# Performance work log

Measured on AMD Instinct MI355X. Metric: run time of the kernel, lower is better.

Reference implementation:

```python
import jax, jax.numpy as jnp
import numpy as np

N_QUBITS = 12
N_LAYERS = 3
HID = 16
IN_DIM = 6
BATCH = 4096
C64 = jnp.complex64


def _ry(t):
    c = jnp.cos(t / 2).astype(C64)
    s = jnp.sin(t / 2).astype(C64)
    return jnp.stack([jnp.stack([c, -s], -1), jnp.stack([s, c], -1)], -2)


def _rx(t):
    c = jnp.cos(t / 2).astype(C64)
    s = jnp.sin(t / 2).astype(C64)
    js = 1j * s
    return jnp.stack([jnp.stack([c, -js], -1), jnp.stack([-js, c], -1)], -2)


def _rz(t):
    e = jnp.exp(-1j * t.astype(C64) / 2)
    z = jnp.zeros_like(e)
    return jnp.stack([jnp.stack([e, z], -1), jnp.stack([z, jnp.conj(e)], -1)], -2)


def _apply_1q(state, U, wire):
    # state: (B,) + (2,)*n ; U: (2,2) shared or (B,2,2) per-sample
    s = jnp.moveaxis(state, wire + 1, 1)
    if U.ndim == 2:
        s = jnp.einsum('ij,bj...->bi...', U, s)
    else:
        s = jnp.einsum('bij,bj...->bi...', U, s)
    return jnp.moveaxis(s, 1, wire + 1)


def _cnot(state, c, t):
    ax_c = c + 1
    s0 = jnp.take(state, 0, axis=ax_c)
    s1 = jnp.take(state, 1, axis=ax_c)
    t_ax = t + 1 if t < c else t  # target axis after removing control axis
    s1 = jnp.flip(s1, axis=t_ax)  # X on target when control=1
    return jnp.stack([s0, s1], axis=ax_c)


def _quantum(angles, qparams):
    # angles: (B, n_qubits) angle-encoding RY rotations; qparams: (L, n, 3)
    B = angles.shape[0]
    n = N_QUBITS
    state = jnp.zeros((B,) + (2,) * n, C64).at[(slice(None),) + (0,) * n].set(1.0)
    for i in range(n):
        state = _apply_1q(state, _ry(angles[:, i]), i)
    for l in range(N_LAYERS):
        for i in range(n):
            # RX then RY then RZ on wire i -> fused 2x2
            U = _rz(qparams[l, i, 2]) @ _ry(qparams[l, i, 1]) @ _rx(qparams[l, i, 0])
            state = _apply_1q(state, U, i)
        for i in range(n - 1):
            state = _cnot(state, i, i + 1)
        if n > 2:
            state = _cnot(state, n - 1, 0)
    p = state.real ** 2 + state.imag ** 2  # (B,) + (2,)*n
    evs = []
    for i in range(n):
        axes = tuple(a for a in range(1, n + 1) if a != i + 1)
        pi = p.sum(axes)  # (B, 2)
        evs.append(pi[:, 0] - pi[:, 1])
    return jnp.stack(evs, axis=1)  # (B, n) PauliZ expvals


def setup_inputs() -> dict:
    key = jax.random.key(0)
    ks = jax.random.split(key, 14)
    w = lambda k, shape: jax.random.normal(k, shape, jnp.float32) * 0.1
    return {
        'x': jax.random.normal(ks[0], (BATCH, IN_DIM), jnp.float32),
        'W1': w(ks[1], (HID, IN_DIM)), 'b1': w(ks[2], (HID,)),
        'W2': w(ks[3], (HID, HID)), 'b2': w(ks[4], (HID,)),
        'W3': w(ks[5], (N_QUBITS, HID)), 'b3': w(ks[6], (N_QUBITS,)),
        'qparams': w(ks[7], (N_LAYERS, N_QUBITS, 3)),
        'P1': w(ks[8], (HID, N_QUBITS)), 'c1': w(ks[9], (HID,)),
        'P2': w(ks[10], (8, HID)), 'c2': w(ks[11], (8,)),
        'P3': w(ks[12], (1, 8)), 'c3': w(ks[13], (1,)),
    }


def reference(x, W1, b1, W2, b2, W3, b3, qparams, P1, c1, P2, c2, P3, c3):
    # classical preprocessor (dropout = identity at inference)
    h = jax.nn.relu(x @ W1.T + b1)
    h = jax.nn.relu(h @ W2.T + b2)
    angles = h @ W3.T + b3  # (B, n_qubits)
    q = _quantum(angles, qparams)  # (B, n_qubits)
    # classical postprocessor
    o = jax.nn.relu(q @ P1.T + c1)
    o = jax.nn.relu(o @ P2.T + c2)
    o = jax.nn.sigmoid(o @ P3.T + c3)
    return o.squeeze(-1)  # (B,)
```

## Files before the change

### kernel.cpp

```cpp
#include <hip/hip_runtime.h>
#include <stdint.h>

#define NQ   12
#define DIM  4096
#define TPB  256

typedef float   v2f   __attribute__((ext_vector_type(2)));
typedef float   v4f   __attribute__((ext_vector_type(4)));
typedef float   f32x4 __attribute__((ext_vector_type(4)));
typedef _Float16 v2h  __attribute__((ext_vector_type(2)));
typedef _Float16 f16x8 __attribute__((ext_vector_type(8)));
typedef uint32_t u32x4 __attribute__((ext_vector_type(4)));

struct PassP {
  uint16_t v[4];
  uint16_t m[4];
  uint16_t td[4];
  uint8_t  np[8];
  uint8_t  wire[4];
  uint8_t  layer;
  uint8_t  pad[3];
};
struct ROC {
  uint16_t mask[12];
  uint8_t  bin[12];
};

constexpr int chbit(uint32_t x) { int b = -1; for (int i = 0; i < 32; ++i) if ((x >> i) & 1u) b = i; return b; }

constexpr void bmm(uint32_t* C, const uint32_t* A, const uint32_t* B) {
  for (int i = 0; i < NQ; ++i) {
    uint32_t r = 0;
    for (int j = 0; j < NQ; ++j) if ((A[i] >> j) & 1u) r ^= B[j];
    C[i] = r;
  }
}
constexpr void binv(const uint32_t* M, uint32_t* Inv) {
  uint32_t A[NQ] = {}, I[NQ] = {};
  for (int i = 0; i < NQ; ++i) { A[i] = M[i]; I[i] = 1u << i; }
  for (int c = 0; c < NQ; ++c) {
    int piv = -1;
    for (int r = c; r < NQ; ++r) if ((A[r] >> c) & 1u) { piv = r; break; }
    if (piv < 0) continue;
    uint32_t ta = A[c]; A[c] = A[piv]; A[piv] = ta;
    uint32_t ti = I[c]; I[c] = I[piv]; I[piv] = ti;
    for (int r = 0; r < NQ; ++r)
      if (r != c && ((A[r] >> c) & 1u)) { A[r] ^= A[c]; I[r] ^= I[c]; }
  }
  for (int i = 0; i < NQ; ++i) Inv[i] = I[i];
}

constexpr int rank5(const uint32_t* cols, int n) {
  uint32_t rows[5] = {}; int rnk = 0;
  for (int q = 0; q < n; ++q) {
    uint32_t x = cols[q] & 31u;
    for (int bit = 4; bit >= 0; --bit) {
      if (!((x >> bit) & 1u)) continue;
      if (rows[bit]) { x ^= rows[bit]; }
      else { rows[bit] = x; ++rnk; break; }
    }
  }
  return rnk;
}
constexpr int penalty(int r) {
  return r >= 5 ? 0 : r == 4 ? 58 : r == 3 ? 194 : r == 2 ? 469 : 1100;
}

constexpr PassP make_pass(int p) {
  PassP pp{};
  uint32_t A[NQ] = {}; A[0] = 0xFFEu;
  for (int i = 1; i < NQ; ++i) A[i] = (1u << (i + 1)) - 1u;
  uint32_t A2[NQ] = {}, Ai[NQ] = {}, A2i[NQ] = {};
  bmm(A2, A, A);
  binv(A, Ai); binv(A2, A2i);

  const int L = (p < 3) ? 1 : 2;
  const int wb = (p % 3) * 4;
  const uint32_t* M  = (L == 1) ? A  : A2;
  const uint32_t* Mi = (L == 1) ? Ai : A2i;
  uint32_t v0[4] = {}, m0[4] = {};
  for (int i = 0; i < 4; ++i) {
    int w = wb + i; uint32_t col = 0;
    for (int r = 0; r < NQ; ++r) col |= ((Mi[r] >> w) & 1u) << r;
    v0[i] = col; m0[i] = M[w];
  }
  uint32_t Bc[NQ] = {};
  for (int b = 0; b < NQ; ++b) {
    uint32_t col = 1u << b;
    for (int i = 0; i < 4; ++i) if ((m0[i] >> b) & 1u) col ^= v0[i];
    Bc[b] = col;
  }
  uint32_t redv[4] = {}; int pbit[4] = {}; uint32_t pivmask = 0;
  for (int i = 0; i < 4; ++i) {
    redv[i] = v0[i];
    for (int k2 = 0; k2 < i; ++k2) if ((redv[i] >> pbit[k2]) & 1u) redv[i] ^= redv[k2];
    pbit[i] = chbit(redv[i]); pivmask |= 1u << pbit[i];
  }
  uint8_t np0[8] = {}; int nc = 0;
  for (int b = 0; b < NQ; ++b) if (!((pivmask >> b) & 1u)) np0[nc++] = (uint8_t)b;

  int bestCost = 1 << 30;
  int bsel[4] = {0, 1, 2, 3}; int bperm[4] = {0, 1, 2, 3};
  for (int a = 0; a < 8; ++a) for (int b = a + 1; b < 8; ++b)
  for (int c = b + 1; c < 8; ++c) for (int d = c + 1; d < 8; ++d) {
    uint32_t jc[4] = {Bc[np0[a]], Bc[np0[b]], Bc[np0[c]], Bc[np0[d]]};
    int prk[4][4] = {};
    for (int i = 0; i < 4; ++i)
      for (int j = i + 1; j < 4; ++j) {
        uint32_t sp[6] = {jc[0], jc[1], jc[2], jc[3], v0[i], v0[j]};
        prk[i][j] = prk[j][i] = rank5(sp, 6);
      }
    for (int pa = 0; pa < 4; ++pa) for (int pb2 = 0; pb2 < 4; ++pb2) {
      if (pb2 == pa) continue;
      for (int pc = 0; pc < 4; ++pc) {
        if (pc == pa || pc == pb2) continue;
        const int pd = 6 - pa - pb2 - pc;
        const int cost = penalty(prk[pc][pd]) + penalty(prk[pb2][pc]);
        if (cost < bestCost) {
          bestCost = cost;
          bsel[0] = a; bsel[1] = b; bsel[2] = c; bsel[3] = d;
          bperm[0] = pa; bperm[1] = pb2; bperm[2] = pc; bperm[3] = pd;
        }
      }
    }
  }
  int rem[4] = {}; int rc2 = 0;
  for (int q = 0; q < 8; ++q)
    if (q != bsel[0] && q != bsel[1] && q != bsel[2] && q != bsel[3]) rem[rc2++] = q;

  uint8_t npn[8] = {};
  npn[0] = np0[bsel[0]]; npn[1] = np0[bsel[1]];
  npn[2] = np0[bsel[2]]; npn[3] = np0[bsel[3]];
  npn[4] = np0[rem[0]]; npn[5] = np0[rem[1]];
  npn[6] = np0[rem[2]]; npn[7] = np0[rem[3]];
  for (int q = 0; q < 8; ++q) pp.np[q] = npn[q];
  for (int i = 0; i < 4; ++i) {
    pp.v[i] = (uint16_t)v0[bperm[i]];
    pp.m[i] = (uint16_t)m0[bperm[i]];
    pp.wire[i] = (uint8_t)(wb + bperm[i]);
  }
  pp.td[0] = 0;
  pp.td[1] = (uint16_t)Bc[npn[4]];
  pp.td[2] = (uint16_t)Bc[npn[5]];
  pp.td[3] = (uint16_t)(Bc[npn[4]] ^ Bc[npn[5]]);
  pp.layer = (uint8_t)L;
  return pp;
}

constexpr PassP kp0 = make_pass(0);
constexpr PassP kp1 = make_pass(1);
constexpr PassP kp2 = make_pass(2);
constexpr PassP kp3 = make_pass(3);
constexpr PassP kp4 = make_pass(4);
constexpr PassP kp5 = make_pass(5);

template<int P>
constexpr PassP pget() {
  if constexpr (P == 0) return kp0;
  else if constexpr (P == 1) return kp1;
  else if constexpr (P == 2) return kp2;
  else if constexpr (P == 3) return kp3;
  else if constexpr (P == 4) return kp4;
  else return kp5;
}

constexpr ROC make_ro() {
  ROC r{};
  uint32_t A[NQ] = {}; A[0] = 0xFFEu;
  for (int i = 1; i < NQ; ++i) A[i] = (1u << (i + 1)) - 1u;
  uint32_t A2[NQ] = {}, A3[NQ] = {};
  bmm(A2, A, A); bmm(A3, A2, A);
  for (int i = 0; i < NQ; ++i) r.mask[i] = (uint16_t)A3[i];
  for (int i = 0; i < NQ; ++i) {
    uint32_t b = 0;
    b |= (uint32_t)(__builtin_popcount(A3[i] & (uint32_t)kp5.v[0]) & 1) << 0;
    b |= (uint32_t)(__builtin_popcount(A3[i] & (uint32_t)kp5.v[3]) & 1) << 1;
    b |= (uint32_t)(__builtin_popcount(A3[i] & (uint32_t)kp5.td[1]) & 1) << 2;
    b |= (uint32_t)(__builtin_popcount(A3[i] & (uint32_t)kp5.td[2]) & 1) << 3;
    r.bin[i] = (uint8_t)b;
  }
  return r;
}
constexpr ROC roc = make_ro();

__device__ __forceinline__ v2f cmulf(v2f a, v2f b) {
  return (v2f){a.x * b.x - a.y * b.y, a.x * b.y + a.y * b.x};
}
__device__ __forceinline__ uint32_t f2h2(float a, float b) {
  return __builtin_bit_cast(uint32_t, __builtin_amdgcn_cvt_pkrtz(a, b));
}
__device__ __forceinline__ uint32_t pk_rtn(float a, float b) {
  v2h h = {(_Float16)a, (_Float16)b};
  return __builtin_bit_cast(uint32_t, h);
}

__device__ __forceinline__ void build_u(const float* __restrict__ qp, int l, int w, float U[8]) {
  float p0 = qp[(l * 12 + w) * 3 + 0];
  float p1 = qp[(l * 12 + w) * 3 + 1];
  float p2 = qp[(l * 12 + w) * 3 + 2];
  float cx, sx, cy, sy, cz, sz;
  sincosf(0.5f * p0, &sx, &cx);
  sincosf(0.5f * p1, &sy, &cy);
  sincosf(0.5f * p2, &sz, &cz);
  float M00x =  cy * cx, M00y =  sy * sx;
  float M01x = -sy * cx, M01y = -cy * sx;
  float M10x =  sy * cx, M10y = -cy * sx;
  float M11x =  cy * cx, M11y = -sy * sx;
  U[0] = cz * M00x + sz * M00y; U[1] = cz * M00y - sz * M00x;
  U[2] = cz * M01x + sz * M01y; U[3] = cz * M01y - sz * M01x;
  U[4] = cz * M10x - sz * M10y; U[5] = cz * M10y + sz * M10x;
  U[6] = cz * M11x - sz * M11y; U[7] = cz * M11y + sz * M11x;
}

__device__ __forceinline__ int am_col(int c, int i) {
  return ((((c >> 2) ^ ((i >> 1) & 3)) << 2) | (c & 3));
}

template<int P>
__device__ __forceinline__ void build_am_g(uint32_t* __restrict__ Am_g,
                                           const v2f (*gg)[12][4], int t) {
  constexpr PassP pp = pget<P>();
  const int r_ = t >> 4, c_ = t & 15;
  v2f e = (v2f){1.f, 0.f};
  #pragma unroll
  for (int i = 0; i < 4; ++i) {
    v2f u = gg[pp.layer - 1][pp.wire[i]][(((r_ >> i) & 1) << 1) | ((c_ >> i) & 1)];
    e = cmulf(e, u);
  }
  const int ra = 2 * r_, rb = 2 * r_ + 1;
  Am_g[P * 512 + ra * 16 + am_col(c_, ra)] = pk_rtn(e.x, -e.y);
  Am_g[P * 512 + rb * 16 + am_col(c_, rb)] = pk_rtn(e.y, e.x);
}

__global__ __launch_bounds__(256) void prep_kernel(const float* __restrict__ qp,
                                                   uint32_t* __restrict__ Am_g,
                                                   float* __restrict__ U0_g) {
  __shared__ v2f gg[2][12][4];
  const int t = threadIdx.x;
  if (t < 24) {
    const int L = t / 12 + 1, w = t % 12;
    float U[8]; build_u(qp, L, w, U);
    gg[L - 1][w][0] = (v2f){U[0], U[1]};
    gg[L - 1][w][1] = (v2f){U[2], U[3]};
    gg[L - 1][w][2] = (v2f){U[4], U[5]};
    gg[L - 1][w][3] = (v2f){U[6], U[7]};
  } else if (t >= 32 && t < 44) {
    const int w = t - 32;
    float U[8]; build_u(qp, 0, w, U);
    #pragma unroll
    for (int k = 0; k < 8; ++k) U0_g[w * 8 + k] = U[k];
  }
  __syncthreads();
  build_am_g<0>(Am_g, gg, t);
  build_am_g<1>(Am_g, gg, t);
  build_am_g<2>(Am_g, gg, t);
  build_am_g<3>(Am_g, gg, t);
  build_am_g<4>(Am_g, gg, t);
  build_am_g<5>(Am_g, gg, t);
}

template<int P, bool LAST>
__device__ __forceinline__ void do_pass(uint32_t* st, f16x8 a0, f16x8 a1,
                                        int t, float* ev) {
  constexpr PassP pp = pget<P>();
  const int lane = t & 63;
  const int wv   = t >> 6;
  const int g    = lane >> 4;
  const int t6 = (lane & 15) | (wv << 6);
  int rep = 0;
  #pragma unroll
  for (int k = 0; k < 8; ++k) rep |= ((t6 >> k) & 1) << pp.np[k];
  int base = rep;
  #pragma unroll
  for (int i = 0; i < 4; ++i)
    if (__popc(pp.m[i] & rep) & 1) base ^= pp.v[i];
  const int cgr = ((g & 1) ? pp.v[2] : 0) ^ ((g & 2) ? pp.v[3] : 0);
  const int cgw = ((g & 1) ? pp.v[1] : 0) ^ ((g & 2) ? pp.v[2] : 0);
  float pr[16];
  const f32x4 z = {0.f, 0.f, 0.f, 0.f};
  #pragma unroll
  for (int T = 0; T < 4; ++T) {
    const int bT = base ^ pp.td[T];
    const int ra = bT ^ cgr;
    u32x4 braw = { st[ra], st[ra ^ pp.v[0]], st[ra ^ pp.v[1]],
                   st[ra ^ (pp.v[0] ^ pp.v[1])] };
    f16x8 bf = __builtin_bit_cast(f16x8, braw);
    f32x4 c0 = __builtin_amdgcn_mfma_f32_16x16x32_f16(a0, bf, z, 0, 0, 0);
    f32x4 c1 = __builtin_amdgcn_mfma_f32_16x16x32_f16(a1, bf, z, 0, 0, 0);
    if constexpr (!LAST) {
      const int wa = bT ^ cgw;
      st[wa]                       = f2h2(c0.x, c0.y);
      st[wa ^ pp.v[0]]             = f2h2(c0.z, c0.w);
      st[wa ^ pp.v[3]]             = f2h2(c1.x, c1.y);
      st[wa ^ (pp.v[3] ^ pp.v[0])] = f2h2(c1.z, c1.w);
    } else {
      const int nb = ((T & 1) << 2) | ((T >> 1) << 3);
      pr[nb]     = c0.x * c0.x + c0.y * c0.y;
      pr[nb | 1] = c0.z * c0.z + c0.w * c0.w;
      pr[nb | 2] = c1.x * c1.x + c1.y * c1.y;
      pr[nb | 3] = c1.z * c1.z + c1.w * c1.w;
    }
  }
  if constexpr (LAST) {
    #pragma unroll
    for (int gs = 1; gs < 16; gs <<= 1) {
      #pragma unroll
      for (int j = 0; j < 16; ++j) {
        if (j & gs) continue;
        float u = pr[j], w2 = pr[j | gs];
        pr[j] = u + w2; pr[j | gs] = u - w2;
      }
    }
    const int baseL = base ^ cgw;
    #pragma unroll
    for (int i = 0; i < NQ; ++i) {
      float h = pr[roc.bin[i]];
      int s = (__popc(roc.mask[i] & baseL) & 1) << 31;
      ev[i] = __int_as_float(__float_as_int(h) ^ s);
    }
  }
}

#define LDA(P, A0, A1) {                                                        \
  const int li_ = lane & 15;                                                    \
  const int q_  = g ^ ((li_ >> 1) & 3);                                         \
  A0 = __builtin_bit_cast(f16x8,                                                \
      *reinterpret_cast<const u32x4*>(Am_g + (P) * 512 + li_ * 16 + q_ * 4));   \
  A1 = __builtin_bit_cast(f16x8,                                                \
      *reinterpret_cast<const u32x4*>(Am_g + (P) * 512 + (li_ + 16) * 16 + q_ * 4)); \
}

__global__ __launch_bounds__(TPB, 8) void hqc_kernel(
    const float* __restrict__ x,  const float* __restrict__ W1, const float* __restrict__ b1,
    const float* __restrict__ W2, const float* __restrict__ b2,
    const float* __restrict__ W3, const float* __restrict__ b3,
    const float* __restrict__ P1, const float* __restrict__ c1,
    const float* __restrict__ P2, const float* __restrict__ c2,
    const float* __restrict__ P3, const float* __restrict__ c3,
    const uint32_t* __restrict__ Am_g, const float* __restrict__ U0_g,
    float* __restrict__ out)
{
  __shared__ uint32_t st[DIM];
  __shared__ v4f  gpk0[12][2];
  __shared__ float red[4][NQ];

  const int s    = blockIdx.x;
  const int t    = threadIdx.x;
  const int lane = t & 63;
  const int wv   = t >> 6;
  const int g    = lane >> 4;

  f16x8 a0c, a1c, a0n, a1n;
  LDA(0, a0c, a1c)

  if (wv == 0 && lane < 16) {
    float a = b1[lane];
    #pragma unroll
    for (int k = 0; k < 6; ++k) a = fmaf(W1[lane * 6 + k], x[s * 6 + k], a);
    float h1 = fmaxf(a, 0.f);
    float a2 = b2[lane];
    #pragma unroll
    for (int k = 0; k < 16; ++k) a2 = fmaf(W2[lane * 16 + k], __shfl(h1, k, 64), a2);
    float h2 = fmaxf(a2, 0.f);
    const int lw = (lane < NQ) ? lane : 0;
    float a3 = b3[lw];
    #pragma unroll
    for (int k = 0; k < 16; ++k) a3 = fmaf(W3[lw * 16 + k], __shfl(h2, k, 64), a3);
    if (lane < NQ) {
      const float* u = U0_g + lane * 8;
      float ca, sa; sincosf(0.5f * a3, &sa, &ca);
      float c0x = u[0] * ca + u[2] * sa, c0y = u[1] * ca + u[3] * sa;
      float c1x = u[4] * ca + u[6] * sa, c1y = u[5] * ca + u[7] * sa;
      gpk0[lane][0] = (v4f){c0x, c0x, -c0y, c0y};
      gpk0[lane][1] = (v4f){c1x, c1x, -c1y, c1y};
    }
  }
  __syncthreads();

  {
    v2f acc = (v2f){1.f, 0.f};
    #pragma unroll
    for (int i = 0; i < 8; ++i) {
      v4f gk = gpk0[i][(t >> i) & 1];
      acc = gk.xy * acc + gk.zw * acc.yx;
    }
    v2f l16[16];
    l16[0] = acc;
    #pragma unroll
    for (int i = 0; i < 4; ++i) {
      v4f g0 = gpk0[8 + i][0], g1 = gpk0[8 + i][1];
      #pragma unroll
      for (int j = 0; j < (1 << i); ++j) {
        v2f a = l16[j];
        l16[j | (1 << i)] = g1.xy * a + g1.zw * a.yx;
        l16[j]            = g0.xy * a + g0.zw * a.yx;
      }
    }
    #pragma unroll
    for (int j = 0; j < 16; ++j) st[t | (j << 8)] = f2h2(l16[j].x, l16[j].y);
  }
  __syncthreads();

  float ev[NQ];
  LDA(1, a0n, a1n)
  do_pass<0, false>(st, a0c, a1c, t, ev); __syncthreads();
  a0c = a0n; a1c = a1n; LDA(2, a0n, a1n)
  do_pass<1, false>(st, a0c, a1c, t, ev); __syncthreads();
  a0c = a0n; a1c = a1n; LDA(3, a0n, a1n)
  do_pass<2, false>(st, a0c, a1c, t, ev); __syncthreads();
  a0c = a0n; a1c = a1n; LDA(4, a0n, a1n)
  do_pass<3, false>(st, a0c, a1c, t, ev); __syncthreads();
  a0c = a0n; a1c = a1n; LDA(5, a0n, a1n)
  do_pass<4, false>(st, a0c, a1c, t, ev); __syncthreads();
  a0c = a0n; a1c = a1n;
  do_pass<5, true >(st, a0c, a1c, t, ev);

  #pragma unroll
  for (int off = 32; off >= 1; off >>= 1) {
    #pragma unroll
    for (int i = 0; i < NQ; ++i) ev[i] += __shfl_xor(ev[i], off, 64);
  }
  if (lane == 0) {
    #pragma unroll
    for (int i = 0; i < NQ; ++i) red[wv][i] = ev[i];
  }
  __syncthreads();

  if (wv == 0 && lane < 16) {
    float q = (lane < NQ)
      ? (red[0][lane] + red[1][lane] + red[2][lane] + red[3][lane])
      : 0.f;
    float a = c1[lane];
    #pragma unroll
    for (int j = 0; j < NQ; ++j) a = fmaf(P1[lane * NQ + j], __shfl(q, j, 64), a);
    float o1 = fmaxf(a, 0.f);
    float a2 = c2[lane & 7];
    #pragma unroll
    for (int j = 0; j < 16; ++j) a2 = fmaf(P2[(lane & 7) * 16 + j], __shfl(o1, j, 64), a2);
    float o2 = fmaxf(a2, 0.f);
    float a3 = c3[0];
    #pragma unroll
    for (int j = 0; j < 8; ++j) a3 = fmaf(P3[j], __shfl(o2, j, 64), a3);
    if (lane == 0) out[s] = 1.f / (1.f + expf(-a3));
  }
}

extern "C" void kernel_launch(void* const* d_in, const int* in_sizes, int n_in,
                              void* d_out, int out_size, void* d_ws, size_t ws_size,
                              hipStream_t stream) {
  (void)in_sizes; (void)n_in; (void)ws_size;
  uint32_t* Am_g = (uint32_t*)d_ws;
  float*    U0_g = (float*)((char*)d_ws + 6 * 512 * 4);
  const float* qp = (const float*)d_in[7];
  prep_kernel<<<1, 256, 0, stream>>>(qp, Am_g, U0_g);
  hqc_kernel<<<out_size, TPB, 0, stream>>>(
      (const float*)d_in[0],  (const float*)d_in[1],  (const float*)d_in[2],
      (const float*)d_in[3],  (const float*)d_in[4],  (const float*)d_in[5],
      (const float*)d_in[6],
      (const float*)d_in[8],  (const float*)d_in[9],
      (const float*)d_in[10], (const float*)d_in[11],
      (const float*)d_in[12], (const float*)d_in[13],
      Am_g, U0_g,
      (float*)d_out);
}
```

Before: 56.37 us.

## Permute state storage so each MFMA pass reads contiguous 16-byte LDS vectors

```diff
diff --git a/kernel.cpp b/kernel.cpp
--- a/kernel.cpp
+++ b/kernel.cpp
@@ -12,21 +12,23 @@
 typedef _Float16 f16x8 __attribute__((ext_vector_type(8)));
 typedef uint32_t u32x4 __attribute__((ext_vector_type(4)));
 
-struct PassP {
-  uint16_t v[4];
-  uint16_t m[4];
-  uint16_t td[4];
+struct PassL {
+  uint32_t v[4], m[4];
+  uint32_t Be[8];
   uint8_t  np[8];
-  uint8_t  wire[4];
-  uint8_t  layer;
-  uint8_t  pad[3];
+  uint8_t  layer, wb;
 };
-struct ROC {
-  uint16_t mask[12];
-  uint8_t  bin[12];
+struct PassC {
+  uint16_t WD[8];
+  uint16_t WQ1, WQ2;
+  uint16_t WV0, WV3;
+  uint16_t SM[12];
+  uint8_t  robin[12];
+  uint8_t  layer, wb;
 };
-
-constexpr int chbit(uint32_t x) { int b = -1; for (int i = 0; i < 32; ++i) if ((x >> i) & 1u) b = i; return b; }
+struct InitC { uint16_t ICt[8]; uint16_t ICj[16]; };
+
+constexpr int par(uint32_t x) { return __builtin_popcount(x) & 1; }
 
 constexpr void bmm(uint32_t* C, const uint32_t* A, const uint32_t* B) {
   for (int i = 0; i < NQ; ++i) {
@@ -49,7 +51,6 @@
   }
   for (int i = 0; i < NQ; ++i) Inv[i] = I[i];
 }
-
 constexpr int rank5(const uint32_t* cols, int n) {
   uint32_t rows[5] = {}; int rnk = 0;
   for (int q = 0; q < n; ++q) {
@@ -62,126 +63,173 @@
   }
   return rnk;
 }
-constexpr int penalty(int r) {
-  return r >= 5 ? 0 : r == 4 ? 58 : r == 3 ? 194 : r == 2 ? 469 : 1100;
-}
-
-constexpr PassP make_pass(int p) {
-  PassP pp{};
+
+constexpr PassL passL_default(int p) {
+  PassL L{};
   uint32_t A[NQ] = {}; A[0] = 0xFFEu;
   for (int i = 1; i < NQ; ++i) A[i] = (1u << (i + 1)) - 1u;
   uint32_t A2[NQ] = {}, Ai[NQ] = {}, A2i[NQ] = {};
-  bmm(A2, A, A);
-  binv(A, Ai); binv(A2, A2i);
-
-  const int L = (p < 3) ? 1 : 2;
-  const int wb = (p % 3) * 4;
-  const uint32_t* M  = (L == 1) ? A  : A2;
-  const uint32_t* Mi = (L == 1) ? Ai : A2i;
-  uint32_t v0[4] = {}, m0[4] = {};
+  bmm(A2, A, A); binv(A, Ai); binv(A2, A2i);
+  const int Lr = (p < 3) ? 1 : 2, wb = (p % 3) * 4;
+  const uint32_t* M  = (Lr == 1) ? A  : A2;
+  const uint32_t* Mi = (Lr == 1) ? Ai : A2i;
   for (int i = 0; i < 4; ++i) {
-    int w = wb + i; uint32_t col = 0;
+    const int w = wb + i; uint32_t col = 0;
     for (int r = 0; r < NQ; ++r) col |= ((Mi[r] >> w) & 1u) << r;
-    v0[i] = col; m0[i] = M[w];
+    L.v[i] = col; L.m[i] = M[w];
   }
   uint32_t Bc[NQ] = {};
   for (int b = 0; b < NQ; ++b) {
     uint32_t col = 1u << b;
-    for (int i = 0; i < 4; ++i) if ((m0[i] >> b) & 1u) col ^= v0[i];
+    for (int i = 0; i < 4; ++i) if ((L.m[i] >> b) & 1u) col ^= L.v[i];
     Bc[b] = col;
   }
-  uint32_t redv[4] = {}; int pbit[4] = {}; uint32_t pivmask = 0;
+  uint32_t redv[4] = {}; uint32_t pivmask = 0;
   for (int i = 0; i < 4; ++i) {
-    redv[i] = v0[i];
-    for (int k2 = 0; k2 < i; ++k2) if ((redv[i] >> pbit[k2]) & 1u) redv[i] ^= redv[k2];
-    pbit[i] = chbit(redv[i]); pivmask |= 1u << pbit[i];
-  }
-  uint8_t np0[8] = {}; int nc = 0;
-  for (int b = 0; b < NQ; ++b) if (!((pivmask >> b) & 1u)) np0[nc++] = (uint8_t)b;
-
-  int bestCost = 1 << 30;
-  int bsel[4] = {0, 1, 2, 3}; int bperm[4] = {0, 1, 2, 3};
-  for (int a = 0; a < 8; ++a) for (int b = a + 1; b < 8; ++b)
-  for (int c = b + 1; c < 8; ++c) for (int d = c + 1; d < 8; ++d) {
-    uint32_t jc[4] = {Bc[np0[a]], Bc[np0[b]], Bc[np0[c]], Bc[np0[d]]};
-    int prk[4][4] = {};
-    for (int i = 0; i < 4; ++i)
-      for (int j = i + 1; j < 4; ++j) {
-        uint32_t sp[6] = {jc[0], jc[1], jc[2], jc[3], v0[i], v0[j]};
-        prk[i][j] = prk[j][i] = rank5(sp, 6);
-      }
-    for (int pa = 0; pa < 4; ++pa) for (int pb2 = 0; pb2 < 4; ++pb2) {
-      if (pb2 == pa) continue;
-      for (int pc = 0; pc < 4; ++pc) {
-        if (pc == pa || pc == pb2) continue;
-        const int pd = 6 - pa - pb2 - pc;
-        const int cost = penalty(prk[pc][pd]) + penalty(prk[pb2][pc]);
-        if (cost < bestCost) {
-          bestCost = cost;
-          bsel[0] = a; bsel[1] = b; bsel[2] = c; bsel[3] = d;
-          bperm[0] = pa; bperm[1] = pb2; bperm[2] = pc; bperm[3] = pd;
-        }
-      }
-    }
-  }
-  int rem[4] = {}; int rc2 = 0;
-  for (int q = 0; q < 8; ++q)
-    if (q != bsel[0] && q != bsel[1] && q != bsel[2] && q != bsel[3]) rem[rc2++] = q;
-
-  uint8_t npn[8] = {};
-  npn[0] = np0[bsel[0]]; npn[1] = np0[bsel[1]];
-  npn[2] = np0[bsel[2]]; npn[3] = np0[bsel[3]];
-  npn[4] = np0[rem[0]]; npn[5] = np0[rem[1]];
-  npn[6] = np0[rem[2]]; npn[7] = np0[rem[3]];
-  for (int q = 0; q < 8; ++q) pp.np[q] = npn[q];
-  for (int i = 0; i < 4; ++i) {
-    pp.v[i] = (uint16_t)v0[bperm[i]];
-    pp.m[i] = (uint16_t)m0[bperm[i]];
-    pp.wire[i] = (uint8_t)(wb + bperm[i]);
-  }
-  pp.td[0] = 0;
-  pp.td[1] = (uint16_t)Bc[npn[4]];
-  pp.td[2] = (uint16_t)Bc[npn[5]];
-  pp.td[3] = (uint16_t)(Bc[npn[4]] ^ Bc[npn[5]]);
-  pp.layer = (uint8_t)L;
-  return pp;
-}
-
-constexpr PassP kp0 = make_pass(0);
-constexpr PassP kp1 = make_pass(1);
-constexpr PassP kp2 = make_pass(2);
-constexpr PassP kp3 = make_pass(3);
-constexpr PassP kp4 = make_pass(4);
-constexpr PassP kp5 = make_pass(5);
-
-template<int P>
-constexpr PassP pget() {
-  if constexpr (P == 0) return kp0;
-  else if constexpr (P == 1) return kp1;
-  else if constexpr (P == 2) return kp2;
-  else if constexpr (P == 3) return kp3;
-  else if constexpr (P == 4) return kp4;
-  else return kp5;
-}
-
-constexpr ROC make_ro() {
-  ROC r{};
+    redv[i] = L.v[i];
+    for (int k = 0; k < i; ++k) {
+      int pb = 0;
+      for (int b = 0; b < NQ; ++b) if ((redv[k] >> b) & 1u) pb = b;
+      if ((redv[i] >> pb) & 1u) redv[i] ^= redv[k];
+    }
+    int pb = 0;
+    for (int b = 0; b < NQ; ++b) if ((redv[i] >> b) & 1u) pb = b;
+    pivmask |= 1u << pb;
+  }
+  int c = 0;
+  for (int b = 0; b < NQ; ++b)
+    if (!((pivmask >> b) & 1u)) { L.np[c] = (uint8_t)b; L.Be[c] = Bc[b]; ++c; }
+  L.layer = (uint8_t)Lr; L.wb = (uint8_t)wb;
+  return L;
+}
+
+constexpr uint8_t ASSIGN[12] = {0, 1, 6, 7, 2, 3, 4, 5, 8, 9, 10, 11};
+struct Lam { uint32_t minv[NQ]; };
+constexpr Lam make_lam(const PassL& L) {
+  uint32_t bas[12] = {L.v[0], L.v[1], L.v[2], L.v[3],
+                      L.Be[0], L.Be[1], L.Be[2], L.Be[3],
+                      L.Be[4], L.Be[5], L.Be[6], L.Be[7]};
+  uint32_t Mr[NQ] = {};
+  for (int i = 0; i < NQ; ++i) {
+    uint32_t r = 0;
+    for (int j = 0; j < NQ; ++j) r |= ((bas[j] >> i) & 1u) << j;
+    Mr[i] = r;
+  }
+  Lam lm{};
+  binv(Mr, lm.minv);
+  return lm;
+}
+constexpr uint32_t lap(const Lam& lm, uint32_t y) {
+  uint32_t r = 0;
+  for (int j = 0; j < NQ; ++j)
+    if (par(lm.minv[j] & y)) r ^= 1u << ASSIGN[j];
+  return r;
+}
+
+constexpr int P4[24][4] = {
+  {0,1,2,3},{0,1,3,2},{0,2,1,3},{0,2,3,1},{0,3,1,2},{0,3,2,1},
+  {1,0,2,3},{1,0,3,2},{1,2,0,3},{1,2,3,0},{1,3,0,2},{1,3,2,0},
+  {2,0,1,3},{2,0,3,1},{2,1,0,3},{2,1,3,0},{2,3,0,1},{2,3,1,0},
+  {3,0,1,2},{3,0,2,1},{3,1,0,2},{3,1,2,0},{3,2,0,1},{3,2,1,0}};
+
+constexpr PassL reorder_np(const PassL& L, int pi, int s45, int s67) {
+  PassL T = L;
+  for (int k = 0; k < 4; ++k) { T.np[k] = L.np[P4[pi][k]]; T.Be[k] = L.Be[P4[pi][k]]; }
+  if (s45) { T.np[4] = L.np[5]; T.np[5] = L.np[4]; T.Be[4] = L.Be[5]; T.Be[5] = L.Be[4]; }
+  if (s67) { T.np[6] = L.np[7]; T.np[7] = L.np[6]; T.Be[6] = L.Be[7]; T.Be[7] = L.Be[6]; }
+  return T;
+}
+
+constexpr PassL passL_ordered(int p, const PassL& prev) {
+  const PassL L = passL_default(p);
+  int best = -1; PassL bestL = L;
+  for (int pi = 0; pi < 24; ++pi)
+  for (int s45 = 0; s45 < 2; ++s45)
+  for (int s67 = 0; s67 < 2; ++s67) {
+    const PassL T = reorder_np(L, pi, s45, s67);
+    const Lam lm = make_lam(T);
+    uint32_t g[8] = { lap(lm, prev.Be[0]), lap(lm, prev.Be[1]),
+                      lap(lm, prev.Be[2]), lap(lm, prev.Be[3]),
+                      lap(lm, prev.v[1]),  lap(lm, prev.v[2]),
+                      lap(lm, prev.Be[6]), lap(lm, prev.Be[7]) };
+    const int r = rank5(g, 8);
+    if (r > best) { best = r; bestL = T; }
+  }
+  return bestL;
+}
+
+constexpr PassL L0 = passL_default(0);
+constexpr PassL L1 = passL_ordered(1, L0);
+constexpr PassL L2 = passL_ordered(2, L1);
+constexpr PassL L3 = passL_ordered(3, L2);
+constexpr PassL L4 = passL_ordered(4, L3);
+constexpr PassL L5 = passL_ordered(5, L4);
+
+constexpr PassC make_passC(const PassL& L, const PassL& Ln) {
+  PassC c{};
+  const Lam lm = make_lam(Ln);
+  for (int k = 0; k < 8; ++k) c.WD[k] = (uint16_t)lap(lm, L.Be[k]);
+  c.WQ1 = (uint16_t)lap(lm, L.v[1]); c.WQ2 = (uint16_t)lap(lm, L.v[2]);
+  c.WV0 = (uint16_t)lap(lm, L.v[0]); c.WV3 = (uint16_t)lap(lm, L.v[3]);
+  c.layer = L.layer; c.wb = L.wb;
+  return c;
+}
+constexpr PassC make_passC5(const PassL& L) {
+  PassC c{};
   uint32_t A[NQ] = {}; A[0] = 0xFFEu;
   for (int i = 1; i < NQ; ++i) A[i] = (1u << (i + 1)) - 1u;
   uint32_t A2[NQ] = {}, A3[NQ] = {};
   bmm(A2, A, A); bmm(A3, A2, A);
-  for (int i = 0; i < NQ; ++i) r.mask[i] = (uint16_t)A3[i];
   for (int i = 0; i < NQ; ++i) {
-    uint32_t b = 0;
-    b |= (uint32_t)(__builtin_popcount(A3[i] & (uint32_t)kp5.v[0]) & 1) << 0;
-    b |= (uint32_t)(__builtin_popcount(A3[i] & (uint32_t)kp5.v[3]) & 1) << 1;
-    b |= (uint32_t)(__builtin_popcount(A3[i] & (uint32_t)kp5.td[1]) & 1) << 2;
-    b |= (uint32_t)(__builtin_popcount(A3[i] & (uint32_t)kp5.td[2]) & 1) << 3;
-    r.bin[i] = (uint8_t)b;
-  }
-  return r;
-}
-constexpr ROC roc = make_ro();
+    uint32_t sm = 0;
+    sm |= (uint32_t)par(A3[i] & L.Be[0]) << 0;
+    sm |= (uint32_t)par(A3[i] & L.Be[1]) << 1;
+    sm |= (uint32_t)par(A3[i] & L.Be[2]) << 2;
+    sm |= (uint32_t)par(A3[i] & L.Be[3]) << 3;
+    sm |= (uint32_t)par(A3[i] & L.v[1])  << 4;
+    sm |= (uint32_t)par(A3[i] & L.v[2])  << 5;
+    sm |= (uint32_t)par(A3[i] & L.Be[6]) << 6;
+    sm |= (uint32_t)par(A3[i] & L.Be[7]) << 7;
+    c.SM[i] = (uint16_t)sm;
+    uint32_t b = (uint32_t)par(A3[i] & L.v[0])
+               | (uint32_t)par(A3[i] & L.v[3])  << 1
+               | (uint32_t)par(A3[i] & L.Be[4]) << 2
+               | (uint32_t)par(A3[i] & L.Be[5]) << 3;
+    c.robin[i] = (uint8_t)b;
+  }
+  c.layer = L.layer; c.wb = L.wb;
+  return c;
+}
+constexpr InitC make_init(const PassL& L) {
+  InitC ic{};
+  const Lam lm = make_lam(L);
+  for (int b = 0; b < 8; ++b) ic.ICt[b] = (uint16_t)lap(lm, 1u << b);
+  uint32_t Jc[4] = {};
+  for (int b = 0; b < 4; ++b) Jc[b] = lap(lm, 1u << (8 + b));
+  for (int j = 0; j < 16; ++j) {
+    uint32_t r = 0;
+    for (int b = 0; b < 4; ++b) if ((j >> b) & 1) r ^= Jc[b];
+    ic.ICj[j] = (uint16_t)r;
+  }
+  return ic;
+}
+
+constexpr PassC C0 = make_passC(L0, L1);
+constexpr PassC C1 = make_passC(L1, L2);
+constexpr PassC C2 = make_passC(L2, L3);
+constexpr PassC C3 = make_passC(L3, L4);
+constexpr PassC C4 = make_passC(L4, L5);
+constexpr PassC C5 = make_passC5(L5);
+constexpr InitC IC = make_init(L0);
+
+template<int P> constexpr PassC cget() {
+  if constexpr (P == 0) return C0;
+  else if constexpr (P == 1) return C1;
+  else if constexpr (P == 2) return C2;
+  else if constexpr (P == 3) return C3;
+  else if constexpr (P == 4) return C4;
+  else return C5;
+}
 
 __device__ __forceinline__ v2f cmulf(v2f a, v2f b) {
   return (v2f){a.x * b.x - a.y * b.y, a.x * b.y + a.y * b.x};
@@ -193,7 +241,6 @@
   v2h h = {(_Float16)a, (_Float16)b};
   return __builtin_bit_cast(uint32_t, h);
 }
-
 __device__ __forceinline__ void build_u(const float* __restrict__ qp, int l, int w, float U[8]) {
   float p0 = qp[(l * 12 + w) * 3 + 0];
   float p1 = qp[(l * 12 + w) * 3 + 1];
@@ -211,7 +258,6 @@
   U[4] = cz * M10x - sz * M10y; U[5] = cz * M10y + sz * M10x;
   U[6] = cz * M11x - sz * M11y; U[7] = cz * M11y + sz * M11x;
 }
-
 __device__ __forceinline__ int am_col(int c, int i) {
   return ((((c >> 2) ^ ((i >> 1) & 3)) << 2) | (c & 3));
 }
@@ -219,12 +265,12 @@
 template<int P>
 __device__ __forceinline__ void build_am_g(uint32_t* __restrict__ Am_g,
                                            const v2f (*gg)[12][4], int t) {
-  constexpr PassP pp = pget<P>();
+  constexpr PassC pc = cget<P>();
   const int r_ = t >> 4, c_ = t & 15;
   v2f e = (v2f){1.f, 0.f};
   #pragma unroll
   for (int i = 0; i < 4; ++i) {
-    v2f u = gg[pp.layer - 1][pp.wire[i]][(((r_ >> i) & 1) << 1) | ((c_ >> i) & 1)];
+    v2f u = gg[pc.layer - 1][pc.wb + i][(((r_ >> i) & 1) << 1) | ((c_ >> i) & 1)];
     e = cmulf(e, u);
   }
   const int ra = 2 * r_, rb = 2 * r_ + 1;
@@ -262,37 +308,31 @@
 template<int P, bool LAST>
 __device__ __forceinline__ void do_pass(uint32_t* st, f16x8 a0, f16x8 a1,
                                         int t, float* ev) {
-  constexpr PassP pp = pget<P>();
-  const int lane = t & 63;
-  const int wv   = t >> 6;
-  const int g    = lane >> 4;
-  const int t6 = (lane & 15) | (wv << 6);
-  int rep = 0;
-  #pragma unroll
-  for (int k = 0; k < 8; ++k) rep |= ((t6 >> k) & 1) << pp.np[k];
-  int base = rep;
-  #pragma unroll
-  for (int i = 0; i < 4; ++i)
-    if (__popc(pp.m[i] & rep) & 1) base ^= pp.v[i];
-  const int cgr = ((g & 1) ? pp.v[2] : 0) ^ ((g & 2) ? pp.v[3] : 0);
-  const int cgw = ((g & 1) ? pp.v[1] : 0) ^ ((g & 2) ? pp.v[2] : 0);
+  constexpr PassC pc = cget<P>();
+  const int lane = t & 63, wv = t >> 6;
+  const int n = lane & 15, q = lane >> 4;
+  const int rb = (n << 2) | (q << 6) | (wv << 10);
+  int wb_ = 0;
+  if constexpr (!LAST) {
+    wb_ = ((n & 1) ? pc.WD[0] : 0) ^ ((n & 2) ? pc.WD[1] : 0)
+        ^ ((n & 4) ? pc.WD[2] : 0) ^ ((n & 8) ? pc.WD[3] : 0)
+        ^ ((q & 1) ? pc.WQ1 : 0)   ^ ((q & 2) ? pc.WQ2 : 0)
+        ^ ((wv & 1) ? pc.WD[6] : 0) ^ ((wv & 2) ? pc.WD[7] : 0);
+  }
   float pr[16];
   const f32x4 z = {0.f, 0.f, 0.f, 0.f};
   #pragma unroll
   for (int T = 0; T < 4; ++T) {
-    const int bT = base ^ pp.td[T];
-    const int ra = bT ^ cgr;
-    u32x4 braw = { st[ra], st[ra ^ pp.v[0]], st[ra ^ pp.v[1]],
-                   st[ra ^ (pp.v[0] ^ pp.v[1])] };
+    u32x4 braw = *reinterpret_cast<const u32x4*>(&st[rb + (T << 8)]);
     f16x8 bf = __builtin_bit_cast(f16x8, braw);
     f32x4 c0 = __builtin_amdgcn_mfma_f32_16x16x32_f16(a0, bf, z, 0, 0, 0);
     f32x4 c1 = __builtin_amdgcn_mfma_f32_16x16x32_f16(a1, bf, z, 0, 0, 0);
     if constexpr (!LAST) {
-      const int wa = bT ^ cgw;
+      const int wa = wb_ ^ ((T & 1) ? pc.WD[4] : 0) ^ ((T & 2) ? pc.WD[5] : 0);
       st[wa]                       = f2h2(c0.x, c0.y);
-      st[wa ^ pp.v[0]]             = f2h2(c0.z, c0.w);
-      st[wa ^ pp.v[3]]             = f2h2(c1.x, c1.y);
-      st[wa ^ (pp.v[3] ^ pp.v[0])] = f2h2(c1.z, c1.w);
+      st[wa ^ pc.WV0]              = f2h2(c0.z, c0.w);
+      st[wa ^ pc.WV3]              = f2h2(c1.x, c1.y);
+      st[wa ^ (pc.WV0 ^ pc.WV3)]   = f2h2(c1.z, c1.w);
     } else {
       const int nb = ((T & 1) << 2) | ((T >> 1) << 3);
       pr[nb]     = c0.x * c0.x + c0.y * c0.y;
@@ -311,11 +351,11 @@
         pr[j] = u + w2; pr[j | gs] = u - w2;
       }
     }
-    const int baseL = base ^ cgw;
+    const int pw = n | (q << 4) | (wv << 6);
     #pragma unroll
     for (int i = 0; i < NQ; ++i) {
-      float h = pr[roc.bin[i]];
-      int s = (__popc(roc.mask[i] & baseL) & 1) << 31;
+      float h = pr[pc.robin[i]];
+      int s = (__popc(pc.SM[i] & pw) & 1) << 31;
       ev[i] = __int_as_float(__float_as_int(h) ^ s);
     }
   }
@@ -323,7 +363,7 @@
 
 #define LDA(P, A0, A1) {                                                        \
   const int li_ = lane & 15;                                                    \
-  const int q_  = g ^ ((li_ >> 1) & 3);                                         \
+  const int q_  = (lane >> 4) ^ ((li_ >> 1) & 3);                               \
   A0 = __builtin_bit_cast(f16x8,                                                \
       *reinterpret_cast<const u32x4*>(Am_g + (P) * 512 + li_ * 16 + q_ * 4));   \
   A1 = __builtin_bit_cast(f16x8,                                                \
@@ -340,7 +380,7 @@
     const uint32_t* __restrict__ Am_g, const float* __restrict__ U0_g,
     float* __restrict__ out)
 {
-  __shared__ uint32_t st[DIM];
+  __shared__ __align__(16) uint32_t st[DIM];
   __shared__ v4f  gpk0[12][2];
   __shared__ float red[4][NQ];
 
@@ -348,7 +388,6 @@
   const int t    = threadIdx.x;
   const int lane = t & 63;
   const int wv   = t >> 6;
-  const int g    = lane >> 4;
 
   f16x8 a0c, a1c, a0n, a1n;
   LDA(0, a0c, a1c)
@@ -378,6 +417,9 @@
   __syncthreads();
 
   {
+    int tb = 0;
+    #pragma unroll
+    for (int b = 0; b < 8; ++b) if ((t >> b) & 1) tb ^= IC.ICt[b];
     v2f acc = (v2f){1.f, 0.f};
     #pragma unroll
     for (int i = 0; i < 8; ++i) {
@@ -397,7 +439,7 @@
       }
     }
     #pragma unroll
-    for (int j = 0; j < 16; ++j) st[t | (j << 8)] = f2h2(l16[j].x, l16[j].y);
+    for (int j = 0; j < 16; ++j) st[tb ^ IC.ICj[j]] = f2h2(l16[j].x, l16[j].y);
   }
   __syncthreads();
 
```

New measurement: 48.28 us. 1.17x faster.
